# Kernel optimization log

Measured on AMD Instinct MI355X. Metric: run time of the kernel, lower is better.

## Reference

```python
import jax, jax.numpy as jnp
import numpy as np

D_MODEL = 1024
NUM_HEADS = 16
HEAD_DIM = D_MODEL // NUM_HEADS
EPS = 1e-06


def setup_inputs() -> dict:
    key = jax.random.key(0)
    ks = jax.random.split(key, 7)
    B, T, D = 4, 4096, D_MODEL
    scale = 1.0 / np.sqrt(D)
    x = jax.random.normal(ks[0], (B, T, D), dtype=jnp.float32)
    Wq = jax.random.normal(ks[1], (D, D), dtype=jnp.float32) * scale
    Wk = jax.random.normal(ks[2], (D, D), dtype=jnp.float32) * scale
    Wv = jax.random.normal(ks[3], (D, D), dtype=jnp.float32) * scale
    Wo = jax.random.normal(ks[4], (D, D), dtype=jnp.float32) * scale
    Wg = jax.random.normal(ks[5], (D, D), dtype=jnp.float32) * scale
    bg = jnp.zeros((D,), dtype=jnp.float32)
    return {"x": x, "Wq": Wq, "Wk": Wk, "Wv": Wv, "Wo": Wo, "Wg": Wg, "bg": bg}


def phi(x):
    return jax.nn.elu(x) + 1.0


def reference(x, Wq, Wk, Wv, Wo, Wg, bg):
    B, T, D = x.shape
    H, Hd = NUM_HEADS, HEAD_DIM
    # torch nn.Linear: y = x @ W.T
    q = phi((x @ Wq.T).reshape(B, T, H, Hd))
    k = phi((x @ Wk.T).reshape(B, T, H, Hd))
    v = (x @ Wv.T).reshape(B, T, H, Hd)
    k_sum = k.sum(axis=1)                              # [B,H,Hd]
    kv_sum = jnp.einsum('bthd,bthd->bhd', k, v)        # [B,H,Hd] (elementwise-product reduction, as in source)
    # out[b,t,h,v] = sum_d q[b,t,h,d]*kv_sum[b,h,d], identical for every v
    s = jnp.einsum('bthd,bhd->bth', q, kv_sum)         # [B,T,H]
    z = jnp.einsum('bthd,bhd->bth', q, k_sum) + EPS    # [B,T,H]
    out = (s / z)[..., None] * jnp.ones((Hd,), dtype=x.dtype)  # broadcast over head_dim
    out = out.reshape(B, T, D)
    gate = jax.nn.sigmoid(x @ Wg.T + bg)
    return gate * out + (1.0 - gate) * x
```

## Files before the change

kernel.cpp:

```cpp
#include <hip/hip_runtime.h>

#define D_MODEL 1024
#define TSEQ    4096
#define BATCH   4
#define MROWS   (BATCH * TSEQ)
#define KDIM    1024
#define NDIM    1024
#define EPSV    1e-6f

typedef __attribute__((ext_vector_type(8))) short short8;
typedef __attribute__((ext_vector_type(4))) float floatx4;

__device__ inline unsigned short f2bf(float f) {
  unsigned u = __float_as_uint(f);
  unsigned r = (u + 0x7FFFu + ((u >> 16) & 1u)) >> 16;
  return (unsigned short)r;
}
__device__ inline float phi_f(float x) { return x > 0.f ? x + 1.f : __expf(x); }

#define GLD16(gp, lp) __builtin_amdgcn_global_load_lds( \
    (const __attribute__((address_space(1))) void*)(gp), \
    (__attribute__((address_space(3))) void*)(lp), 16, 0, 0)

#define NX4 4194304
#define NW4 262144
#define NZ4 2048

__global__ __launch_bounds__(256) void prep_kernel(
    const float* __restrict__ x,  const float* __restrict__ wq,
    const float* __restrict__ wk, const float* __restrict__ wv,
    const float* __restrict__ wg,
    unsigned short* __restrict__ xb,  unsigned short* __restrict__ wqb,
    unsigned short* __restrict__ wkb, unsigned short* __restrict__ wvb,
    unsigned short* __restrict__ wgb, float* __restrict__ zbase)
{
  long i = (long)blockIdx.x * 256 + threadIdx.x;
  const float* src; unsigned short* dst; long j = i;
  if (j < NX4) { src = x; dst = xb; }
  else {
    j -= NX4;
    if (j < NW4) { src = wq; dst = wqb; }
    else { j -= NW4;
      if (j < NW4) { src = wk; dst = wkb; }
      else { j -= NW4;
        if (j < NW4) { src = wv; dst = wvb; }
        else { j -= NW4;
          if (j < NW4) { src = wg; dst = wgb; }
          else { j -= NW4;
            if (j < NZ4) { float4 zz = {0.f,0.f,0.f,0.f}; ((float4*)zbase)[j] = zz; }
            return;
          }
        }
      }
    }
  }
  float4 f = ((const float4*)src)[j];
  ushort4 o;
  o.x = f2bf(f.x); o.y = f2bf(f.y); o.z = f2bf(f.z); o.w = f2bf(f.w);
  ((ushort4*)dst)[j] = o;
}

#define BM 256
#define BN 128
#define BK 64
#define NSTEP (KDIM / BK)


__global__ __launch_bounds__(512, 1) void gemm_kv_kernel(
    const unsigned short* __restrict__ A,
    const unsigned short* __restrict__ Wk, const unsigned short* __restrict__ Wv,
    float* __restrict__ ksum, float* __restrict__ kvsum)
{
  __shared__ __align__(16) unsigned short As0[BM * BK], As1[BM * BK];
  __shared__ __align__(16) unsigned short Bk0[BN * BK], Bk1[BN * BK];
  __shared__ __align__(16) unsigned short Bv0[BN * BK], Bv1[BN * BK];

  const int bid = blockIdx.x;
  const int sw  = (bid & 7) * 64 + (bid >> 3);
  const int bn  = sw & 7;
  const int bm  = sw >> 3;

  const int tid  = threadIdx.x;
  const int lane = tid & 63;
  const int w    = tid >> 6;
  const int wr   = (w >> 2) * 128;
  const int wc   = (w & 3) * 32;
  const int la   = lane & 15;
  const int l4   = lane >> 4;

  floatx4 ak[8][2], av[8][2];
#pragma unroll
  for (int i = 0; i < 8; i++)
#pragma unroll
    for (int j = 0; j < 2; j++) {
      floatx4 zz = {0.f,0.f,0.f,0.f}; ak[i][j] = zz; av[i][j] = zz;
    }

  const unsigned short* Ablk = A  + (size_t)bm * BM * KDIM;
  const unsigned short* Bkb  = Wk + (size_t)bn * BN * KDIM;
  const unsigned short* Bvb  = Wv + (size_t)bn * BN * KDIM;

  auto stage_half = [&](unsigned short* Aw, unsigned short* Bkw, unsigned short* Bvw,
                        int kt, int half) {
#pragma unroll
    for (int j = 0; j < 2; ++j) {
      int s = tid + (half * 2 + j) * 512;
      int row = s >> 3, sl = s & 7;
      size_t g = (size_t)row * KDIM + kt + ((sl ^ (row & 7)) << 3);
      GLD16(Ablk + g, Aw + (size_t)s * 8);
    }
    {
      int s = tid + half * 512;
      int row = s >> 3, sl = s & 7;
      size_t g = (size_t)row * KDIM + kt + ((sl ^ (row & 7)) << 3);
      GLD16(Bkb + g, Bkw + (size_t)s * 8);
      GLD16(Bvb + g, Bvw + (size_t)s * 8);
    }
  };

  auto kstep = [&](const unsigned short* Ar, const unsigned short* Bkr,
                   const unsigned short* Bvr,
                   unsigned short* Aw, unsigned short* Bkw, unsigned short* Bvw,
                   int ktn, bool pre) {
    short8 bkf[2][2], bvf[2][2];
#pragma unroll
    for (int p = 0; p < 4; ++p) {
      short8 af[2][2];
#pragma unroll
      for (int rp = 0; rp < 2; ++rp)
#pragma unroll
        for (int kk = 0; kk < 2; ++kk) {
          int row  = wr + (2 * p + rp) * 16 + la;
          int slot = kk * 4 + l4;
          af[rp][kk] = *(const short8*)(Ar + row * BK + ((slot ^ (row & 7)) << 3));
        }
      if (p == 0) {
#pragma unroll
        for (int j = 0; j < 2; ++j)
#pragma unroll
          for (int kk = 0; kk < 2; ++kk) {
            int row  = wc + j * 16 + la;
            int slot = kk * 4 + l4;
            int off  = row * BK + ((slot ^ (row & 7)) << 3);
            bkf[j][kk] = *(const short8*)(Bkr + off);
            bvf[j][kk] = *(const short8*)(Bvr + off);
          }
      }
      if (p == 0 && pre) stage_half(Aw, Bkw, Bvw, ktn, 0);
      if (p == 1 && pre) stage_half(Aw, Bkw, Bvw, ktn, 1);
      __builtin_amdgcn_s_barrier();
      __builtin_amdgcn_s_setprio(1);
#pragma unroll
      for (int rp = 0; rp < 2; ++rp)
#pragma unroll
        for (int j = 0; j < 2; ++j)
#pragma unroll
          for (int kk = 0; kk < 2; ++kk) {
            ak[2*p+rp][j] = __builtin_amdgcn_mfma_f32_16x16x32_bf16(
                af[rp][kk], bkf[j][kk], ak[2*p+rp][j], 0, 0, 0);
            av[2*p+rp][j] = __builtin_amdgcn_mfma_f32_16x16x32_bf16(
                af[rp][kk], bvf[j][kk], av[2*p+rp][j], 0, 0, 0);
          }
      __builtin_amdgcn_s_setprio(0);
      if (p == 3) asm volatile("s_waitcnt vmcnt(0)" ::: "memory");
      __builtin_amdgcn_s_barrier();
    }
  };

  stage_half(As0, Bk0, Bv0, 0, 0);
  stage_half(As0, Bk0, Bv0, 0, 1);
  asm volatile("s_waitcnt vmcnt(0)" ::: "memory");
  __builtin_amdgcn_s_barrier();

  for (int st2 = 0; st2 < NSTEP; st2 += 2) {
    kstep(As0, Bk0, Bv0, As1, Bk1, Bv1, (st2 + 1) * BK, true);
    kstep(As1, Bk1, Bv1, As0, Bk0, Bv0, (st2 + 2) * BK, st2 + 2 < NSTEP);
  }

  const int b = bm >> 4;
  float kp[2] = {0.f, 0.f};
  float vp[2] = {0.f, 0.f};
#pragma unroll
  for (int j = 0; j < 2; j++)
#pragma unroll
    for (int mi = 0; mi < 8; mi++)
#pragma unroll
      for (int r = 0; r < 4; r++) {
        float kk = phi_f(ak[mi][j][r]);
        kp[j] += kk;
        vp[j] += kk * av[mi][j][r];
      }
#pragma unroll
  for (int j = 0; j < 2; j++) {
    kp[j] += __shfl_xor(kp[j], 16, 64); kp[j] += __shfl_xor(kp[j], 32, 64);
    vp[j] += __shfl_xor(vp[j], 16, 64); vp[j] += __shfl_xor(vp[j], 32, 64);
  }
  if (lane < 16) {
#pragma unroll
    for (int j = 0; j < 2; j++) {
      int col = bn * BN + wc + j * 16 + lane;
      atomicAdd(ksum  + (size_t)b * D_MODEL + col, kp[j]);
      atomicAdd(kvsum + (size_t)b * D_MODEL + col, vp[j]);
    }
  }
}

__global__ __launch_bounds__(512, 1) void gemm_qg_kernel(
    const unsigned short* __restrict__ A,
    const unsigned short* __restrict__ Wq, const unsigned short* __restrict__ Wg,
    const float* __restrict__ x, const float* __restrict__ bg,
    const float* __restrict__ ksum, const float* __restrict__ kvsum,
    float* __restrict__ out)
{
  __shared__ __align__(16) unsigned short As0[BM * BK], As1[BM * BK];
  __shared__ __align__(16) unsigned short Bq0[BN * BK], Bq1[BN * BK];
  __shared__ __align__(16) unsigned short Bg0[BN * BK], Bg1[BN * BK];
  __shared__ float o_lds[2 * BM];

  const int bid = blockIdx.x;
  const int sw  = (bid & 7) * 64 + (bid >> 3);
  const int bn  = sw & 7;
  const int bm  = sw >> 3;

  const int tid  = threadIdx.x;
  const int lane = tid & 63;
  const int w    = tid >> 6;
  const int is_g = w >> 2;
  const int wl   = w & 3;
  const int wr   = (wl >> 1) * 128;
  const int wc   = (wl & 1) * 64;
  const int la   = lane & 15;
  const int l4   = lane >> 4;

  floatx4 acc[8][4];
#pragma unroll
  for (int i = 0; i < 8; i++)
#pragma unroll
    for (int j = 0; j < 4; j++) { floatx4 zz = {0.f,0.f,0.f,0.f}; acc[i][j] = zz; }

  const unsigned short* Ablk = A  + (size_t)bm * BM * KDIM;
  const unsigned short* Bqb  = Wq + (size_t)bn * BN * KDIM;
  const unsigned short* Bgb  = Wg + (size_t)bn * BN * KDIM;

  auto stage_half = [&](unsigned short* Aw, unsigned short* Bqw, unsigned short* Bgw,
                        int kt, int half) {
#pragma unroll
    for (int j = 0; j < 2; ++j) {
      int s = tid + (half * 2 + j) * 512;
      int row = s >> 3, sl = s & 7;
      size_t g = (size_t)row * KDIM + kt + ((sl ^ (row & 7)) << 3);
      GLD16(Ablk + g, Aw + (size_t)s * 8);
    }
    {
      int s = tid + half * 512;
      int row = s >> 3, sl = s & 7;
      size_t g = (size_t)row * KDIM + kt + ((sl ^ (row & 7)) << 3);
      GLD16(Bqb + g, Bqw + (size_t)s * 8);
      GLD16(Bgb + g, Bgw + (size_t)s * 8);
    }
  };

  auto kstep = [&](const unsigned short* Ar, const unsigned short* Bqr,
                   const unsigned short* Bgr,
                   unsigned short* Aw, unsigned short* Bqw, unsigned short* Bgw,
                   int ktn, bool pre) {
    const unsigned short* Br = is_g ? Bgr : Bqr;
    short8 bf[4][2];
#pragma unroll
    for (int p = 0; p < 4; ++p) {
      short8 af[2][2];
#pragma unroll
      for (int rp = 0; rp < 2; ++rp)
#pragma unroll
        for (int kk = 0; kk < 2; ++kk) {
          int row  = wr + (2 * p + rp) * 16 + la;
          int slot = kk * 4 + l4;
          af[rp][kk] = *(const short8*)(Ar + row * BK + ((slot ^ (row & 7)) << 3));
        }
      if (p == 0) {
#pragma unroll
        for (int j = 0; j < 4; ++j)
#pragma unroll
          for (int kk = 0; kk < 2; ++kk) {
            int row  = wc + j * 16 + la;
            int slot = kk * 4 + l4;
            bf[j][kk] = *(const short8*)(Br + row * BK + ((slot ^ (row & 7)) << 3));
          }
      }
      if (p == 0 && pre) stage_half(Aw, Bqw, Bgw, ktn, 0);
      if (p == 1 && pre) stage_half(Aw, Bqw, Bgw, ktn, 1);
      __builtin_amdgcn_s_barrier();
      __builtin_amdgcn_s_setprio(1);
#pragma unroll
      for (int rp = 0; rp < 2; ++rp)
#pragma unroll
        for (int j = 0; j < 4; ++j)
#pragma unroll
          for (int kk = 0; kk < 2; ++kk)
            acc[2*p+rp][j] = __builtin_amdgcn_mfma_f32_16x16x32_bf16(
                af[rp][kk], bf[j][kk], acc[2*p+rp][j], 0, 0, 0);
      __builtin_amdgcn_s_setprio(0);
      if (p == 3) asm volatile("s_waitcnt vmcnt(0)" ::: "memory");
      __builtin_amdgcn_s_barrier();
    }
  };

  stage_half(As0, Bq0, Bg0, 0, 0);
  stage_half(As0, Bq0, Bg0, 0, 1);
  asm volatile("s_waitcnt vmcnt(0)" ::: "memory");
  __builtin_amdgcn_s_barrier();

  for (int st2 = 0; st2 < NSTEP; st2 += 2) {
    kstep(As0, Bq0, Bg0, As1, Bq1, Bg1, (st2 + 1) * BK, true);
    kstep(As1, Bq1, Bg1, As0, Bq0, Bg0, (st2 + 2) * BK, st2 + 2 < NSTEP);
  }

  const int b  = bm >> 4;
  const int ro = l4 * 4;
  const int co = la;
  const int hl = wc >> 6;

  if (!is_g) {
    float kvv[4], ksv[4];
#pragma unroll
    for (int j = 0; j < 4; j++) {
      int col = bn * BN + wc + j * 16 + co;
      kvv[j] = kvsum[(size_t)b * D_MODEL + col];
      ksv[j] = ksum [(size_t)b * D_MODEL + col];
    }
#pragma unroll
    for (int mi = 0; mi < 8; mi++)
#pragma unroll
      for (int r = 0; r < 4; r++) {
        float s = 0.f, z = 0.f;
#pragma unroll
        for (int j = 0; j < 4; j++) {
          float qq = phi_f(acc[mi][j][r]);
          s += qq * kvv[j]; z += qq * ksv[j];
        }
#pragma unroll
        for (int m = 1; m < 16; m <<= 1) {
          s += __shfl_xor(s, m, 64);
          z += __shfl_xor(z, m, 64);
        }
        if (co == 0) o_lds[hl * BM + wr + mi * 16 + ro + r] = s / (z + EPSV);
      }
  }
  __syncthreads();
  if (is_g) {
    float bgv[4];
#pragma unroll
    for (int j = 0; j < 4; j++) bgv[j] = bg[bn * BN + wc + j * 16 + co];
#pragma unroll
    for (int mi = 0; mi < 8; mi++)
#pragma unroll
      for (int r = 0; r < 4; r++) {
        int rowl = wr + mi * 16 + ro + r;
        int grow = bm * BM + rowl;
        float ov = o_lds[hl * BM + rowl];
#pragma unroll
        for (int j = 0; j < 4; j++) {
          int gcol = bn * BN + wc + j * 16 + co;
          float gt = 1.f / (1.f + __expf(-(acc[mi][j][r] + bgv[j])));
          float xv = x[(size_t)grow * D_MODEL + gcol];
          out[(size_t)grow * D_MODEL + gcol] = gt * ov + (1.f - gt) * xv;
        }
      }
  }
}

extern "C" void kernel_launch(void* const* d_in, const int* in_sizes, int n_in,
                              void* d_out, int out_size, void* d_ws, size_t ws_size,
                              hipStream_t stream) {
  (void)in_sizes; (void)n_in; (void)out_size; (void)ws_size;
  const float* x  = (const float*)d_in[0];
  const float* Wq = (const float*)d_in[1];
  const float* Wk = (const float*)d_in[2];
  const float* Wv = (const float*)d_in[3];
  const float* Wg = (const float*)d_in[5];
  const float* bg = (const float*)d_in[6];
  float* out = (float*)d_out;

  char* ws = (char*)d_ws;
  const size_t xel = (size_t)MROWS * D_MODEL;
  const size_t wel = (size_t)NDIM * KDIM;
  unsigned short* xbf = (unsigned short*)ws; ws += xel * 2;
  unsigned short* wqb = (unsigned short*)ws; ws += wel * 2;
  unsigned short* wkb = (unsigned short*)ws; ws += wel * 2;
  unsigned short* wvb = (unsigned short*)ws; ws += wel * 2;
  unsigned short* wgb = (unsigned short*)ws; ws += wel * 2;
  float* ksum  = (float*)ws; ws += (size_t)BATCH * D_MODEL * 4;
  float* kvsum = (float*)ws; ws += (size_t)BATCH * D_MODEL * 4;

  const long total4 = (long)NX4 + 4L * NW4 + NZ4;
  prep_kernel<<<(int)((total4 + 255) / 256), 256, 0, stream>>>(
      x, Wq, Wk, Wv, Wg, xbf, wqb, wkb, wvb, wgb, ksum);

  gemm_kv_kernel<<<512, 512, 0, stream>>>(xbf, wkb, wvb, ksum, kvsum);

  gemm_qg_kernel<<<512, 512, 0, stream>>>(xbf, wqb, wgb, x, bg, ksum, kvsum, out);
}
```

Measured before the change: 278.5 us.

## Deepen GEMM prefetch to two stages in flight with partial vmcnt waits

Both fused GEMM kernels now issue the loads for the next two K-tiles up front and wait with vmcnt(8), leaving one tile's loads in flight instead of draining every load each step. Staging moves out of the MFMA phases to after each buffer is consumed. Load offsets and swizzled LDS slot indices are precomputed to cut address arithmetic. The aim is to hide global-to-LDS latency better, at the cost of relying on exact vmcnt accounting and on extra barriers.

```diff
diff --git a/kernel.cpp b/kernel.cpp
--- a/kernel.cpp
+++ b/kernel.cpp
@@ -21,6 +21,9 @@
 #define GLD16(gp, lp) __builtin_amdgcn_global_load_lds( \
     (const __attribute__((address_space(1))) void*)(gp), \
     (__attribute__((address_space(3))) void*)(lp), 16, 0, 0)
+
+#define VMCNT8() asm volatile("s_waitcnt vmcnt(8)" ::: "memory")
+#define VMCNT0() asm volatile("s_waitcnt vmcnt(0)" ::: "memory")
 
 #define NX4 4194304
 #define NW4 262144
@@ -65,7 +68,6 @@
 #define BK 64
 #define NSTEP (KDIM / BK)
 
-
 __global__ __launch_bounds__(512, 1) void gemm_kv_kernel(
     const unsigned short* __restrict__ A,
     const unsigned short* __restrict__ Wk, const unsigned short* __restrict__ Wv,
@@ -100,54 +102,55 @@
   const unsigned short* Bkb  = Wk + (size_t)bn * BN * KDIM;
   const unsigned short* Bvb  = Wv + (size_t)bn * BN * KDIM;
 
-  auto stage_half = [&](unsigned short* Aw, unsigned short* Bkw, unsigned short* Bvw,
-                        int kt, int half) {
-#pragma unroll
-    for (int j = 0; j < 2; ++j) {
-      int s = tid + (half * 2 + j) * 512;
-      int row = s >> 3, sl = s & 7;
-      size_t g = (size_t)row * KDIM + kt + ((sl ^ (row & 7)) << 3);
-      GLD16(Ablk + g, Aw + (size_t)s * 8);
-    }
-    {
-      int s = tid + half * 512;
-      int row = s >> 3, sl = s & 7;
-      size_t g = (size_t)row * KDIM + kt + ((sl ^ (row & 7)) << 3);
-      GLD16(Bkb + g, Bkw + (size_t)s * 8);
-      GLD16(Bvb + g, Bvw + (size_t)s * 8);
+  int aoff[4], boff[2];
+#pragma unroll
+  for (int i = 0; i < 4; i++) {
+    int s = tid + i * 512; int r = s >> 3;
+    aoff[i] = r * KDIM + (((s & 7) ^ (r & 7)) << 3);
+  }
+#pragma unroll
+  for (int i = 0; i < 2; i++) {
+    int s = tid + i * 512; int r = s >> 3;
+    boff[i] = r * KDIM + (((s & 7) ^ (r & 7)) << 3);
+  }
+
+  auto stage8 = [&](unsigned short* Aw, unsigned short* Bkw, unsigned short* Bvw,
+                    int kt) {
+#pragma unroll
+    for (int i = 0; i < 4; ++i)
+      GLD16(Ablk + aoff[i] + kt, Aw + (size_t)(tid + i * 512) * 8);
+#pragma unroll
+    for (int i = 0; i < 2; ++i) {
+      GLD16(Bkb + boff[i] + kt, Bkw + (size_t)(tid + i * 512) * 8);
+      GLD16(Bvb + boff[i] + kt, Bvw + (size_t)(tid + i * 512) * 8);
     }
   };
 
-  auto kstep = [&](const unsigned short* Ar, const unsigned short* Bkr,
-                   const unsigned short* Bvr,
-                   unsigned short* Aw, unsigned short* Bkw, unsigned short* Bvw,
-                   int ktn, bool pre) {
+  const int sl0 = (0 * 4 + l4) ^ (la & 7);
+  const int sl1 = (1 * 4 + l4) ^ (la & 7);
+
+  auto kphases = [&](const unsigned short* Ar, const unsigned short* Bkr,
+                     const unsigned short* Bvr) {
     short8 bkf[2][2], bvf[2][2];
 #pragma unroll
     for (int p = 0; p < 4; ++p) {
       short8 af[2][2];
 #pragma unroll
-      for (int rp = 0; rp < 2; ++rp)
-#pragma unroll
-        for (int kk = 0; kk < 2; ++kk) {
-          int row  = wr + (2 * p + rp) * 16 + la;
-          int slot = kk * 4 + l4;
-          af[rp][kk] = *(const short8*)(Ar + row * BK + ((slot ^ (row & 7)) << 3));
-        }
+      for (int rp = 0; rp < 2; ++rp) {
+        int row = wr + (2 * p + rp) * 16 + la;
+        af[rp][0] = *(const short8*)(Ar + row * BK + sl0 * 8);
+        af[rp][1] = *(const short8*)(Ar + row * BK + sl1 * 8);
+      }
       if (p == 0) {
 #pragma unroll
-        for (int j = 0; j < 2; ++j)
-#pragma unroll
-          for (int kk = 0; kk < 2; ++kk) {
-            int row  = wc + j * 16 + la;
-            int slot = kk * 4 + l4;
-            int off  = row * BK + ((slot ^ (row & 7)) << 3);
-            bkf[j][kk] = *(const short8*)(Bkr + off);
-            bvf[j][kk] = *(const short8*)(Bvr + off);
-          }
-      }
-      if (p == 0 && pre) stage_half(Aw, Bkw, Bvw, ktn, 0);
-      if (p == 1 && pre) stage_half(Aw, Bkw, Bvw, ktn, 1);
+        for (int j = 0; j < 2; ++j) {
+          int row = wc + j * 16 + la;
+          bkf[j][0] = *(const short8*)(Bkr + row * BK + sl0 * 8);
+          bkf[j][1] = *(const short8*)(Bkr + row * BK + sl1 * 8);
+          bvf[j][0] = *(const short8*)(Bvr + row * BK + sl0 * 8);
+          bvf[j][1] = *(const short8*)(Bvr + row * BK + sl1 * 8);
+        }
+      }
       __builtin_amdgcn_s_barrier();
       __builtin_amdgcn_s_setprio(1);
 #pragma unroll
@@ -162,19 +165,28 @@
                 af[rp][kk], bvf[j][kk], av[2*p+rp][j], 0, 0, 0);
           }
       __builtin_amdgcn_s_setprio(0);
-      if (p == 3) asm volatile("s_waitcnt vmcnt(0)" ::: "memory");
       __builtin_amdgcn_s_barrier();
     }
   };
 
-  stage_half(As0, Bk0, Bv0, 0, 0);
-  stage_half(As0, Bk0, Bv0, 0, 1);
-  asm volatile("s_waitcnt vmcnt(0)" ::: "memory");
+  stage8(As0, Bk0, Bv0, 0);
+  stage8(As1, Bk1, Bv1, BK);
+  VMCNT8();
   __builtin_amdgcn_s_barrier();
 
   for (int st2 = 0; st2 < NSTEP; st2 += 2) {
-    kstep(As0, Bk0, Bv0, As1, Bk1, Bv1, (st2 + 1) * BK, true);
-    kstep(As1, Bk1, Bv1, As0, Bk0, Bv0, (st2 + 2) * BK, st2 + 2 < NSTEP);
+    kphases(As0, Bk0, Bv0);
+    if (st2 + 2 < NSTEP) { stage8(As0, Bk0, Bv0, (st2 + 2) * BK); VMCNT8(); }
+    else                 { VMCNT0(); }
+    __builtin_amdgcn_s_barrier();
+    kphases(As1, Bk1, Bv1);
+    if (st2 + 3 < NSTEP) {
+      stage8(As1, Bk1, Bv1, (st2 + 3) * BK); VMCNT8();
+      __builtin_amdgcn_s_barrier();
+    } else if (st2 + 2 < NSTEP) {
+      VMCNT0();
+      __builtin_amdgcn_s_barrier();
+    }
   }
 
   const int b = bm >> 4;
@@ -242,53 +254,52 @@
   const unsigned short* Bqb  = Wq + (size_t)bn * BN * KDIM;
   const unsigned short* Bgb  = Wg + (size_t)bn * BN * KDIM;
 
-  auto stage_half = [&](unsigned short* Aw, unsigned short* Bqw, unsigned short* Bgw,
-                        int kt, int half) {
-#pragma unroll
-    for (int j = 0; j < 2; ++j) {
-      int s = tid + (half * 2 + j) * 512;
-      int row = s >> 3, sl = s & 7;
-      size_t g = (size_t)row * KDIM + kt + ((sl ^ (row & 7)) << 3);
-      GLD16(Ablk + g, Aw + (size_t)s * 8);
-    }
-    {
-      int s = tid + half * 512;
-      int row = s >> 3, sl = s & 7;
-      size_t g = (size_t)row * KDIM + kt + ((sl ^ (row & 7)) << 3);
-      GLD16(Bqb + g, Bqw + (size_t)s * 8);
-      GLD16(Bgb + g, Bgw + (size_t)s * 8);
+  int aoff[4], boff[2];
+#pragma unroll
+  for (int i = 0; i < 4; i++) {
+    int s = tid + i * 512; int r = s >> 3;
+    aoff[i] = r * KDIM + (((s & 7) ^ (r & 7)) << 3);
+  }
+#pragma unroll
+  for (int i = 0; i < 2; i++) {
+    int s = tid + i * 512; int r = s >> 3;
+    boff[i] = r * KDIM + (((s & 7) ^ (r & 7)) << 3);
+  }
+
+  auto stage8 = [&](unsigned short* Aw, unsigned short* Bqw, unsigned short* Bgw,
+                    int kt) {
+#pragma unroll
+    for (int i = 0; i < 4; ++i)
+      GLD16(Ablk + aoff[i] + kt, Aw + (size_t)(tid + i * 512) * 8);
+#pragma unroll
+    for (int i = 0; i < 2; ++i) {
+      GLD16(Bqb + boff[i] + kt, Bqw + (size_t)(tid + i * 512) * 8);
+      GLD16(Bgb + boff[i] + kt, Bgw + (size_t)(tid + i * 512) * 8);
     }
   };
 
-  auto kstep = [&](const unsigned short* Ar, const unsigned short* Bqr,
-                   const unsigned short* Bgr,
-                   unsigned short* Aw, unsigned short* Bqw, unsigned short* Bgw,
-                   int ktn, bool pre) {
-    const unsigned short* Br = is_g ? Bgr : Bqr;
+  const int sl0 = (0 * 4 + l4) ^ (la & 7);
+  const int sl1 = (1 * 4 + l4) ^ (la & 7);
+
+  auto kphases = [&](const unsigned short* Ar, const unsigned short* Br) {
     short8 bf[4][2];
 #pragma unroll
     for (int p = 0; p < 4; ++p) {
       short8 af[2][2];
 #pragma unroll
-      for (int rp = 0; rp < 2; ++rp)
-#pragma unroll
-        for (int kk = 0; kk < 2; ++kk) {
-          int row  = wr + (2 * p + rp) * 16 + la;
-          int slot = kk * 4 + l4;
-          af[rp][kk] = *(const short8*)(Ar + row * BK + ((slot ^ (row & 7)) << 3));
-        }
+      for (int rp = 0; rp < 2; ++rp) {
+        int row = wr + (2 * p + rp) * 16 + la;
+        af[rp][0] = *(const short8*)(Ar + row * BK + sl0 * 8);
+        af[rp][1] = *(const short8*)(Ar + row * BK + sl1 * 8);
+      }
       if (p == 0) {
 #pragma unroll
-        for (int j = 0; j < 4; ++j)
-#pragma unroll
-          for (int kk = 0; kk < 2; ++kk) {
-            int row  = wc + j * 16 + la;
-            int slot = kk * 4 + l4;
-            bf[j][kk] = *(const short8*)(Br + row * BK + ((slot ^ (row & 7)) << 3));
-          }
-      }
-      if (p == 0 && pre) stage_half(Aw, Bqw, Bgw, ktn, 0);
-      if (p == 1 && pre) stage_half(Aw, Bqw, Bgw, ktn, 1);
+        for (int j = 0; j < 4; ++j) {
+          int row = wc + j * 16 + la;
+          bf[j][0] = *(const short8*)(Br + row * BK + sl0 * 8);
+          bf[j][1] = *(const short8*)(Br + row * BK + sl1 * 8);
+        }
+      }
       __builtin_amdgcn_s_barrier();
       __builtin_amdgcn_s_setprio(1);
 #pragma unroll
@@ -300,19 +311,28 @@
             acc[2*p+rp][j] = __builtin_amdgcn_mfma_f32_16x16x32_bf16(
                 af[rp][kk], bf[j][kk], acc[2*p+rp][j], 0, 0, 0);
       __builtin_amdgcn_s_setprio(0);
-      if (p == 3) asm volatile("s_waitcnt vmcnt(0)" ::: "memory");
       __builtin_amdgcn_s_barrier();
     }
   };
 
-  stage_half(As0, Bq0, Bg0, 0, 0);
-  stage_half(As0, Bq0, Bg0, 0, 1);
-  asm volatile("s_waitcnt vmcnt(0)" ::: "memory");
+  stage8(As0, Bq0, Bg0, 0);
+  stage8(As1, Bq1, Bg1, BK);
+  VMCNT8();
   __builtin_amdgcn_s_barrier();
 
   for (int st2 = 0; st2 < NSTEP; st2 += 2) {
-    kstep(As0, Bq0, Bg0, As1, Bq1, Bg1, (st2 + 1) * BK, true);
-    kstep(As1, Bq1, Bg1, As0, Bq0, Bg0, (st2 + 2) * BK, st2 + 2 < NSTEP);
+    kphases(As0, is_g ? Bg0 : Bq0);
+    if (st2 + 2 < NSTEP) { stage8(As0, Bq0, Bg0, (st2 + 2) * BK); VMCNT8(); }
+    else                 { VMCNT0(); }
+    __builtin_amdgcn_s_barrier();
+    kphases(As1, is_g ? Bg1 : Bq1);
+    if (st2 + 3 < NSTEP) {
+      stage8(As1, Bq1, Bg1, (st2 + 3) * BK); VMCNT8();
+      __builtin_amdgcn_s_barrier();
+    } else if (st2 + 2 < NSTEP) {
+      VMCNT0();
+      __builtin_amdgcn_s_barrier();
+    }
   }
 
   const int b  = bm >> 4;
```

Result: slower. 298.6 us (+7.2%).
